# Kernel tuning notes

Hardware: AMD Instinct MI355X
Metric: run time of the kernel (lower is better)

## Reference

```python
import jax, jax.numpy as jnp
import numpy as np

N_NODES = 50000
N_EDGES = 1600000
N_DECODE = 500000
D = 128
EPS = 1e-6


def _sage_conv(x, src, dst, Wl, bl, Wr, n_nodes):
    # PyG SAGEConv (mean aggr): out = lin_l(mean_{j in N(i)} x_j) + lin_r(x_i)
    msg = x[src]                                            # [E, D] gather
    s = jax.ops.segment_sum(msg, dst, num_segments=n_nodes) # [N, D]
    cnt = jax.ops.segment_sum(jnp.ones((src.shape[0],), x.dtype), dst,
                              num_segments=n_nodes)         # [N]
    aggr = s / jnp.maximum(cnt, 1.0)[:, None]
    return aggr @ Wl + bl + x @ Wr


def setup_inputs() -> dict:
    key = jax.random.key(0)
    ks = jax.random.split(key, 9)
    scale = 1.0 / np.sqrt(D)
    x = jax.random.normal(ks[0], (N_NODES, D), dtype=jnp.float32)
    edge_index = jax.random.randint(ks[1], (2, N_EDGES), 0, N_NODES, dtype=jnp.int64)
    decode_index = jax.random.randint(ks[2], (2, N_DECODE), 0, N_NODES, dtype=jnp.int64)
    W1l = jax.random.normal(ks[3], (D, D), dtype=jnp.float32) * scale
    b1 = jnp.zeros((D,), dtype=jnp.float32)
    W1r = jax.random.normal(ks[4], (D, D), dtype=jnp.float32) * scale
    W2l = jax.random.normal(ks[5], (D, D), dtype=jnp.float32) * scale
    b2 = jnp.zeros((D,), dtype=jnp.float32)
    W2r = jax.random.normal(ks[6], (D, D), dtype=jnp.float32) * scale
    return {"x": x, "edge_index": edge_index, "decode_index": decode_index,
            "W1l": W1l, "b1": b1, "W1r": W1r, "W2l": W2l, "b2": b2, "W2r": W2r}


def reference(x, edge_index, decode_index, W1l, b1, W1r, W2l, b2, W2r):
    src, dst = edge_index[0], edge_index[1]
    h = _sage_conv(x, src, dst, W1l, b1, W1r, N_NODES)
    h = jax.nn.relu(h)
    # dropout is a no-op in eval mode (training=False)
    h = _sage_conv(h, src, dst, W2l, b2, W2r, N_NODES)
    a = h[decode_index[0]]                                  # [Dk, D]
    b = h[decode_index[1]]
    num = jnp.sum(a * b, axis=1)
    denom = jnp.maximum(jnp.linalg.norm(a, axis=1) * jnp.linalg.norm(b, axis=1), EPS)
    return jax.nn.sigmoid(num / denom)
```

## Files before the change

### kernel.cpp

```cpp
#include <hip/hip_runtime.h>
#include <cstddef>

#define D 128
#define NBITS 7
#define BCAP2 6144
#define CHUNK 4096
#define BSTRIDE8 36
#define DNPP 8

typedef float floatx4 __attribute__((ext_vector_type(4)));
typedef float floatx2 __attribute__((ext_vector_type(2)));

__device__ __forceinline__ int incl_scan64(int v) {
    const int lane = threadIdx.x & 63;
#pragma unroll
    for (int o = 1; o < 64; o <<= 1) {
        int u = __shfl_up(v, o);
        if (lane >= o) v += u;
    }
    return v;
}

__device__ __forceinline__ void accf8p(floatx2* a2, uint4 u) {
    unsigned w[4] = {u.x, u.y, u.z, u.w};
#pragma unroll
    for (int k = 0; k < 4; ++k) {
        a2[2 * k + 0] += __builtin_amdgcn_cvt_pk_f32_fp8((int)w[k], false);
        a2[2 * k + 1] += __builtin_amdgcn_cvt_pk_f32_fp8((int)w[k], true);
    }
}

__device__ __forceinline__ float dotf8(uint4 ua, uint4 ub) {
    unsigned wa[4] = {ua.x, ua.y, ua.z, ua.w};
    unsigned wb[4] = {ub.x, ub.y, ub.z, ub.w};
    float dot = 0.f;
#pragma unroll
    for (int k = 0; k < 4; ++k) {
        floatx2 alo = __builtin_amdgcn_cvt_pk_f32_fp8((int)wa[k], false);
        floatx2 ahi = __builtin_amdgcn_cvt_pk_f32_fp8((int)wa[k], true);
        floatx2 blo = __builtin_amdgcn_cvt_pk_f32_fp8((int)wb[k], false);
        floatx2 bhi = __builtin_amdgcn_cvt_pk_f32_fp8((int)wb[k], true);
        dot = fmaf(alo.x, blo.x, dot);
        dot = fmaf(alo.y, blo.y, dot);
        dot = fmaf(ahi.x, bhi.x, dot);
        dot = fmaf(ahi.y, bhi.y, dot);
    }
    return dot;
}

__global__ void __launch_bounds__(256) k1_prep_bucket(
        const float* __restrict__ x, unsigned* __restrict__ xf8,
        int nq, int nblk_a,
        const float* __restrict__ W1l, const float* __restrict__ W1r,
        const float* __restrict__ W2l, const float* __restrict__ W2r,
        unsigned* __restrict__ Wtf8,
        const int* __restrict__ src, const int* __restrict__ dst, int n_edges,
        unsigned* __restrict__ chunk_data, int* __restrict__ chunk_off,
        int nbuck) {
    int blk = (int)blockIdx.x;
    const int tid = threadIdx.x;
    if (blk < nblk_a) {
        int t = blk * 256 + tid;
        if (t < nq) {
            float4 v = ((const float4*)x)[t];
            int lo = __builtin_amdgcn_cvt_pk_fp8_f32(v.x, v.y, 0, false);
            xf8[t] = (unsigned)__builtin_amdgcn_cvt_pk_fp8_f32(v.z, v.w, lo, true);
        }
        return;
    }
    blk -= nblk_a;
    if (blk < 64) {
        int t2 = blk * 256 + tid;
        int widx = t2 >> 12;
        int within = t2 & 4095;
        int n = within >> 5;
        int g = within & 31;
        const float* W = (widx == 0) ? W1l : (widx == 1) ? W1r : (widx == 2) ? W2l : W2r;
        float w0 = W[(size_t)(4 * g + 0) * D + n];
        float w1 = W[(size_t)(4 * g + 1) * D + n];
        float w2 = W[(size_t)(4 * g + 2) * D + n];
        float w3 = W[(size_t)(4 * g + 3) * D + n];
        int lo = __builtin_amdgcn_cvt_pk_fp8_f32(w0, w1, 0, false);
        Wtf8[(size_t)widx * 4096 + (size_t)n * 32 + g] =
            (unsigned)__builtin_amdgcn_cvt_pk_fp8_f32(w2, w3, lo, true);
        return;
    }
    blk -= 64;
    __shared__ int cnt[512];
    __shared__ int cur[512];
    __shared__ int wsum[4];
    __shared__ unsigned ent[CHUNK];
    const int c = blk;
    const int e0 = c * CHUNK;
    const int n = min(CHUNK, n_edges - e0);
    cnt[tid] = 0;
    cnt[tid + 256] = 0;
    __syncthreads();
    for (int i = tid; i < n; i += 256)
        atomicAdd(&cnt[dst[e0 + i] >> NBITS], 1);
    __syncthreads();
    int c0 = cnt[2 * tid], c1 = cnt[2 * tid + 1];
    int v = c0 + c1;
    int s = incl_scan64(v);
    if ((tid & 63) == 63) wsum[tid >> 6] = s;
    __syncthreads();
    {
        int wv = tid >> 6;
        int add = (wv > 0 ? wsum[0] : 0) + (wv > 1 ? wsum[1] : 0) + (wv > 2 ? wsum[2] : 0);
        int excl = s + add - v;
        cur[2 * tid] = excl;
        cur[2 * tid + 1] = excl + c0;
        const size_t base = (size_t)c * (nbuck + 1);
        if (2 * tid <= nbuck) chunk_off[base + 2 * tid] = excl;
        if (2 * tid + 1 <= nbuck) chunk_off[base + 2 * tid + 1] = excl + c0;
    }
    __syncthreads();
    for (int i = tid; i < n; i += 256) {
        int d = dst[e0 + i];
        int sv = src[e0 + i];
        int b = d >> NBITS;
        int p = atomicAdd(&cur[b], 1);
        ent[p] = ((unsigned)(d & ((1 << NBITS) - 1)) << 16) | (unsigned)sv;
    }
    __syncthreads();
    for (int i = tid; i < n; i += 256) chunk_data[(size_t)e0 + i] = ent[i];
}

__global__ void __launch_bounds__(512) k2_csr(
        const unsigned* __restrict__ chunk_data, const int* __restrict__ chunk_off,
        int nchunk, int nbuck,
        unsigned* __restrict__ csr16g, int* __restrict__ offsG,
        int* __restrict__ degG) {
    __shared__ unsigned short lcsr[BCAP2];
    __shared__ int ndeg[128], ncur[128];
    __shared__ int s_w0, s_tot;
    const int tid = threadIdx.x;
    const int b = blockIdx.x;
    const int stride = nbuck + 1;

    if (tid < 128) ndeg[tid] = 0;
    __syncthreads();

    const int w = tid >> 1, half = tid & 1;
    for (int c = w; c < nchunk; c += 256) {
        int beg = chunk_off[(size_t)c * stride + b];
        int end = chunk_off[(size_t)c * stride + b + 1];
        const unsigned* cd = chunk_data + (size_t)c * CHUNK;
        for (int i = beg + half; i < end; i += 2)
            atomicAdd(&ndeg[cd[i] >> 16], 1);
    }
    __syncthreads();
    int v = 0, pd = 0, s = 0;
    if (tid < 128) {
        v = ndeg[tid];
        pd = (v + 7) & ~7;
        s = incl_scan64(pd);
        if (tid == 63) s_w0 = s;
    }
    __syncthreads();
    if (tid < 128) {
        if (tid >= 64) s += s_w0;
        int excl = min(s - pd, BCAP2);
        int de = v;
        if (excl + de > BCAP2) de = max(0, BCAP2 - excl);
        ncur[tid] = excl;
        offsG[(size_t)b * 128 + tid] = excl;
        degG[(size_t)b * 128 + tid] = de;
        if (tid == 127) s_tot = min(s, BCAP2);
    }
    __syncthreads();
    for (int c = w; c < nchunk; c += 256) {
        int beg = chunk_off[(size_t)c * stride + b];
        int end = chunk_off[(size_t)c * stride + b + 1];
        const unsigned* cd = chunk_data + (size_t)c * CHUNK;
        for (int i = beg + half; i < end; i += 2) {
            unsigned e = cd[i];
            int pos = atomicAdd(&ncur[e >> 16], 1);
            if (pos < BCAP2) lcsr[pos] = (unsigned short)(e & 0xffffu);
        }
    }
    __syncthreads();
    {
        int tot = s_tot;
        int words = (tot + 1) >> 1;
        const unsigned* l32 = (const unsigned*)lcsr;
        for (int i = tid; i < words; i += 512)
            csr16g[(size_t)b * (BCAP2 / 2) + i] = l32[i];
    }
}

__global__ void __launch_bounds__(256, 6) gather_hi(
        const unsigned* __restrict__ feat,
        const int* __restrict__ offsG, const int* __restrict__ degG,
        const unsigned* __restrict__ csr16g,
        unsigned* __restrict__ agg, int n_nodes) {
    const int wid = (blockIdx.x * blockDim.x + threadIdx.x) >> 6;
    const int lane = threadIdx.x & 63;
    const int q = lane >> 3;
    const int l8 = lane & 7;
    const int node = wid * 8 + q;
    const int nc = (node < n_nodes) ? node : (n_nodes - 1);
    const unsigned short* csr = (const unsigned short*)csr16g
                                + (size_t)(nc >> NBITS) * BCAP2;
    const int beg = offsG[nc];
    const int de  = degG[nc];
    const int end = beg + de;
    const unsigned* fb = feat + (size_t)l8 * 4;
    floatx2 a2[8];
#pragma unroll
    for (int i = 0; i < 8; ++i) a2[i] = (floatx2)(0.f);
    int e = beg;
    for (; e + 8 <= end; e += 8) {
        uint4 idv = *(const uint4*)(csr + e);
        unsigned id0 = idv.x & 0xffffu, id1 = idv.x >> 16;
        unsigned id2 = idv.y & 0xffffu, id3 = idv.y >> 16;
        unsigned id4 = idv.z & 0xffffu, id5 = idv.z >> 16;
        unsigned id6 = idv.w & 0xffffu, id7 = idv.w >> 16;
        uint4 u0 = *(const uint4*)(fb + (size_t)id0 * 32);
        uint4 u1 = *(const uint4*)(fb + (size_t)id1 * 32);
        uint4 u2 = *(const uint4*)(fb + (size_t)id2 * 32);
        uint4 u3 = *(const uint4*)(fb + (size_t)id3 * 32);
        uint4 u4 = *(const uint4*)(fb + (size_t)id4 * 32);
        uint4 u5 = *(const uint4*)(fb + (size_t)id5 * 32);
        uint4 u6 = *(const uint4*)(fb + (size_t)id6 * 32);
        uint4 u7 = *(const uint4*)(fb + (size_t)id7 * 32);
        accf8p(a2, u0); accf8p(a2, u1); accf8p(a2, u2); accf8p(a2, u3);
        accf8p(a2, u4); accf8p(a2, u5); accf8p(a2, u6); accf8p(a2, u7);
    }
    for (; e < end; ++e) {
        uint4 u0 = *(const uint4*)(fb + (size_t)csr[e] * 32);
        accf8p(a2, u0);
    }
    float r = 1.0f / fmaxf((float)de, 1.0f);
    unsigned o[4];
#pragma unroll
    for (int j = 0; j < 4; ++j) {
        int lo = __builtin_amdgcn_cvt_pk_fp8_f32(a2[2 * j].x * r, a2[2 * j].y * r, 0, false);
        o[j] = (unsigned)__builtin_amdgcn_cvt_pk_fp8_f32(a2[2 * j + 1].x * r,
                                                         a2[2 * j + 1].y * r, lo, true);
    }
    if (node < n_nodes)
        *(uint4*)(agg + (size_t)node * 32 + l8 * 4) = make_uint4(o[0], o[1], o[2], o[3]);
}

__global__ void __launch_bounds__(256, 4) gemm128(
        const unsigned* __restrict__ aggf8, const unsigned* __restrict__ xin8,
        const unsigned* __restrict__ Wt, const float* __restrict__ bias,
        unsigned char* __restrict__ outf8, float* __restrict__ nrm2,
        int n_nodes, int relu) {
    __shared__ unsigned sB[2][128 * BSTRIDE8];
    const int tid = threadIdx.x;
    for (int i = tid; i < 2048; i += 256) {
        int m = i >> 10;
        int col = (i >> 3) & 127;
        int c4 = (i & 7) * 4;
        *(uint4*)&sB[m][col * BSTRIDE8 + c4] =
            *(const uint4*)(Wt + (size_t)m * 4096 + (size_t)col * 32 + c4);
    }
    __syncthreads();

    const int lane = tid & 63;
    const int wv = tid >> 6;
    const int li = lane & 15;
    const int quad = lane >> 4;
    const int node0 = blockIdx.x * 64 + wv * 16;
    if (node0 >= n_nodes) return;

    floatx4 acc[8];
#pragma unroll
    for (int t = 0; t < 8; ++t) acc[t] = (floatx4)(0.f);

    int arow = node0 + li;
    if (arow >= n_nodes) arow = n_nodes - 1;
    const unsigned* ap = aggf8 + (size_t)arow * 32 + quad * 2;
    const unsigned* xp = xin8 + (size_t)arow * 32 + quad * 2;
    const unsigned* sb0 = &sB[0][li * BSTRIDE8 + quad * 2];
    const unsigned* sb1 = &sB[1][li * BSTRIDE8 + quad * 2];

#pragma unroll
    for (int ks = 0; ks < 4; ++ks) {
        long af = *(const long*)(ap + ks * 8);
#pragma unroll
        for (int ct = 0; ct < 8; ++ct) {
            long bf = *(const long*)(sb0 + ct * 16 * BSTRIDE8 + ks * 8);
            acc[ct] = __builtin_amdgcn_mfma_f32_16x16x32_fp8_fp8(af, bf, acc[ct], 0, 0, 0);
        }
    }
#pragma unroll
    for (int ks = 0; ks < 4; ++ks) {
        long af = *(const long*)(xp + ks * 8);
#pragma unroll
        for (int ct = 0; ct < 8; ++ct) {
            long bf = *(const long*)(sb1 + ct * 16 * BSTRIDE8 + ks * 8);
            acc[ct] = __builtin_amdgcn_mfma_f32_16x16x32_fp8_fp8(af, bf, acc[ct], 0, 0, 0);
        }
    }
    float sq[4] = {0.f, 0.f, 0.f, 0.f};
#pragma unroll
    for (int ct = 0; ct < 8; ++ct) {
        int col = ct * 16 + li;
        float bv = bias[col];
#pragma unroll
        for (int r2 = 0; r2 < 4; ++r2) {
            int node2 = node0 + quad * 4 + r2;
            float o = acc[ct][r2] + bv;
            if (relu) o = fmaxf(o, 0.f);
            int pk = __builtin_amdgcn_cvt_pk_fp8_f32(o, o, 0, false);
            if (nrm2) {
                floatx2 dq = __builtin_amdgcn_cvt_pk_f32_fp8(pk, false);
                sq[r2] += dq.x * dq.x;
            }
            if (node2 < n_nodes)
                outf8[(size_t)node2 * D + col] = (unsigned char)(pk & 0xff);
        }
    }
    if (nrm2) {
#pragma unroll
        for (int r2 = 0; r2 < 4; ++r2) {
            float sv = sq[r2];
            sv += __shfl_xor(sv, 1);
            sv += __shfl_xor(sv, 2);
            sv += __shfl_xor(sv, 4);
            sv += __shfl_xor(sv, 8);
            int node2 = node0 + quad * 4 + r2;
            if (li == 0 && node2 < n_nodes) nrm2[node2] = sv;
        }
    }
}

__global__ void __launch_bounds__(256, 4) k5_decode(
        const unsigned* __restrict__ h2, const float* __restrict__ nrm2,
        const int* __restrict__ ia, const int* __restrict__ ib,
        float* __restrict__ out, int n_pairs) {
    const int tid = threadIdx.x;
    const int l8 = tid & 7;
    const int g = blockIdx.x * 32 + (tid >> 3);
    const int strideP = gridDim.x * 32;
    int pa[DNPP], pb[DNPP];
#pragma unroll
    for (int i = 0; i < DNPP; ++i) {
        int p = g + i * strideP;
        int pc = (p < n_pairs) ? p : 0;
        pa[i] = ia[pc];
        pb[i] = ib[pc];
    }
    uint4 ua[DNPP], ub[DNPP];
#pragma unroll
    for (int i = 0; i < DNPP; ++i) {
        ua[i] = *(const uint4*)(h2 + (size_t)pa[i] * 32 + l8 * 4);
        ub[i] = *(const uint4*)(h2 + (size_t)pb[i] * 32 + l8 * 4);
    }
#pragma unroll
    for (int i = 0; i < DNPP; ++i) {
        float dot = dotf8(ua[i], ub[i]);
        dot += __shfl_xor(dot, 1);
        dot += __shfl_xor(dot, 2);
        dot += __shfl_xor(dot, 4);
        int p = g + i * strideP;
        if (l8 == 0 && p < n_pairs) {
            float denom = fmaxf(sqrtf(nrm2[pa[i]] * nrm2[pb[i]]), 1e-6f);
            float s = dot / denom;
            out[p] = 1.0f / (1.0f + expf(-s));
        }
    }
}


extern "C" void kernel_launch(void* const* d_in, const int* in_sizes, int n_in,
                              void* d_out, int out_size, void* d_ws, size_t ws_size,
                              hipStream_t stream) {
    const float* x   = (const float*)d_in[0];
    const int*   ei  = (const int*)d_in[1];
    const int*   di  = (const int*)d_in[2];
    const float* W1l = (const float*)d_in[3];
    const float* b1  = (const float*)d_in[4];
    const float* W1r = (const float*)d_in[5];
    const float* W2l = (const float*)d_in[6];
    const float* b2  = (const float*)d_in[7];
    const float* W2r = (const float*)d_in[8];

    const int N = in_sizes[0] / D;
    const int E = in_sizes[1] / 2;
    const int K = in_sizes[2] / 2;
    const size_t NQ = (size_t)N * 32;
    const int NBUCK = (N + (1 << NBITS) - 1) >> NBITS;
    const int NCHUNK = (E + CHUNK - 1) / CHUNK;

    const int* src  = ei;
    const int* dstp = ei + E;
    const int* dia  = di;
    const int* dib  = di + K;

    unsigned* ws         = (unsigned*)d_ws;
    unsigned* chunk_data = ws;
    int*      chunk_off  = (int*)(chunk_data + E);
    unsigned* csr16g     = (unsigned*)(chunk_off + (size_t)NCHUNK * (NBUCK + 1));
    int*      offsG      = (int*)(csr16g + (size_t)NBUCK * (BCAP2 / 2));
    int*      degG       = offsG + (size_t)NBUCK * 128;
    float*    nrm2       = (float*)(degG + (size_t)NBUCK * 128);
    unsigned* Wtf8       = (unsigned*)(nrm2 + N);
    unsigned* xf8        = Wtf8 + 16384;
    unsigned* h1f8       = xf8 + NQ;
    unsigned* h2f8       = h1f8 + NQ;
    unsigned* aggf8      = h2f8 + NQ;

    float* out = (float*)d_out;

    const int nq = (int)NQ;
    const int nblk_a = (nq + 255) / 256;

    k1_prep_bucket<<<nblk_a + 64 + NCHUNK, 256, 0, stream>>>(
        x, xf8, nq, nblk_a, W1l, W1r, W2l, W2r, Wtf8,
        src, dstp, E, chunk_data, chunk_off, NBUCK);

    k2_csr<<<NBUCK, 512, 0, stream>>>(
        chunk_data, chunk_off, NCHUNK, NBUCK, csr16g, offsG, degG);

    const int gather_blocks = ((N + 7) / 8 + 3) / 4;
    const int gemm_blocks = (N + 63) / 64;

    gather_hi<<<gather_blocks, 256, 0, stream>>>(xf8, offsG, degG, csr16g, aggf8, N);
    gemm128<<<gemm_blocks, 256, 0, stream>>>(aggf8, xf8, Wtf8, b1,
                                             (unsigned char*)h1f8, nullptr, N, 1);

    gather_hi<<<gather_blocks, 256, 0, stream>>>(h1f8, offsG, degG, csr16g, aggf8, N);
    gemm128<<<gemm_blocks, 256, 0, stream>>>(aggf8, h1f8, Wtf8 + 8192, b2,
                                             (unsigned char*)h2f8, nrm2, N, 0);

    {
        int G = (K + 32 * DNPP - 1) / (32 * DNPP);
        k5_decode<<<G, 256, 0, stream>>>(h2f8, nrm2, dia, dib, out, K);
    }
}
```

Measured before the change: 239.9 us.

## Split fp8 feature matrices into two 64-column planes for cache-resident gathers

Stores the fp8 node features (x, h1, h2, agg) as two column planes of 64 bytes per node instead of 128-byte rows. The gather and decode kernels now run once per plane, so each pass touches a 3.2 MB working set that fits better in cache during random neighbor access. The GEMM reads and writes the planar layout, and decode accumulates a partial dot product across two launches. The cost is extra kernel launches, re-reading the CSR indices and decode indices twice, and a byte-strided output store in the GEMM.

```diff
diff --git a/kernel.cpp b/kernel.cpp
--- a/kernel.cpp
+++ b/kernel.cpp
@@ -50,7 +50,7 @@
 
 __global__ void __launch_bounds__(256) k1_prep_bucket(
         const float* __restrict__ x, unsigned* __restrict__ xf8,
-        int nq, int nblk_a,
+        int nq, int nblk_a, int N16,
         const float* __restrict__ W1l, const float* __restrict__ W1r,
         const float* __restrict__ W2l, const float* __restrict__ W2r,
         unsigned* __restrict__ Wtf8,
@@ -64,7 +64,9 @@
         if (t < nq) {
             float4 v = ((const float4*)x)[t];
             int lo = __builtin_amdgcn_cvt_pk_fp8_f32(v.x, v.y, 0, false);
-            xf8[t] = (unsigned)__builtin_amdgcn_cvt_pk_fp8_f32(v.z, v.w, lo, true);
+            unsigned w = (unsigned)__builtin_amdgcn_cvt_pk_fp8_f32(v.z, v.w, lo, true);
+            int n = t >> 5, j = t & 31;
+            xf8[(size_t)(j >> 4) * N16 + (size_t)n * 16 + (j & 15)] = w;
         }
         return;
     }
@@ -189,23 +191,23 @@
     }
 }
 
-__global__ void __launch_bounds__(256, 6) gather_hi(
-        const unsigned* __restrict__ feat,
+__global__ void __launch_bounds__(256, 4) gather_plane(
+        const unsigned* __restrict__ featp,
         const int* __restrict__ offsG, const int* __restrict__ degG,
         const unsigned* __restrict__ csr16g,
-        unsigned* __restrict__ agg, int n_nodes) {
+        unsigned* __restrict__ aggp, int n_nodes) {
     const int wid = (blockIdx.x * blockDim.x + threadIdx.x) >> 6;
     const int lane = threadIdx.x & 63;
-    const int q = lane >> 3;
-    const int l8 = lane & 7;
-    const int node = wid * 8 + q;
+    const int q = lane >> 2;
+    const int l4 = lane & 3;
+    const int node = wid * 16 + q;
     const int nc = (node < n_nodes) ? node : (n_nodes - 1);
     const unsigned short* csr = (const unsigned short*)csr16g
                                 + (size_t)(nc >> NBITS) * BCAP2;
     const int beg = offsG[nc];
     const int de  = degG[nc];
     const int end = beg + de;
-    const unsigned* fb = feat + (size_t)l8 * 4;
+    const unsigned* fb = featp + (size_t)l4 * 4;
     floatx2 a2[8];
 #pragma unroll
     for (int i = 0; i < 8; ++i) a2[i] = (floatx2)(0.f);
@@ -216,19 +218,19 @@
         unsigned id2 = idv.y & 0xffffu, id3 = idv.y >> 16;
         unsigned id4 = idv.z & 0xffffu, id5 = idv.z >> 16;
         unsigned id6 = idv.w & 0xffffu, id7 = idv.w >> 16;
-        uint4 u0 = *(const uint4*)(fb + (size_t)id0 * 32);
-        uint4 u1 = *(const uint4*)(fb + (size_t)id1 * 32);
-        uint4 u2 = *(const uint4*)(fb + (size_t)id2 * 32);
-        uint4 u3 = *(const uint4*)(fb + (size_t)id3 * 32);
-        uint4 u4 = *(const uint4*)(fb + (size_t)id4 * 32);
-        uint4 u5 = *(const uint4*)(fb + (size_t)id5 * 32);
-        uint4 u6 = *(const uint4*)(fb + (size_t)id6 * 32);
-        uint4 u7 = *(const uint4*)(fb + (size_t)id7 * 32);
+        uint4 u0 = *(const uint4*)(fb + (size_t)id0 * 16);
+        uint4 u1 = *(const uint4*)(fb + (size_t)id1 * 16);
+        uint4 u2 = *(const uint4*)(fb + (size_t)id2 * 16);
+        uint4 u3 = *(const uint4*)(fb + (size_t)id3 * 16);
+        uint4 u4 = *(const uint4*)(fb + (size_t)id4 * 16);
+        uint4 u5 = *(const uint4*)(fb + (size_t)id5 * 16);
+        uint4 u6 = *(const uint4*)(fb + (size_t)id6 * 16);
+        uint4 u7 = *(const uint4*)(fb + (size_t)id7 * 16);
         accf8p(a2, u0); accf8p(a2, u1); accf8p(a2, u2); accf8p(a2, u3);
         accf8p(a2, u4); accf8p(a2, u5); accf8p(a2, u6); accf8p(a2, u7);
     }
     for (; e < end; ++e) {
-        uint4 u0 = *(const uint4*)(fb + (size_t)csr[e] * 32);
+        uint4 u0 = *(const uint4*)(fb + (size_t)csr[e] * 16);
         accf8p(a2, u0);
     }
     float r = 1.0f / fmaxf((float)de, 1.0f);
@@ -240,14 +242,14 @@
                                                          a2[2 * j + 1].y * r, lo, true);
     }
     if (node < n_nodes)
-        *(uint4*)(agg + (size_t)node * 32 + l8 * 4) = make_uint4(o[0], o[1], o[2], o[3]);
+        *(uint4*)(aggp + (size_t)node * 16 + l4 * 4) = make_uint4(o[0], o[1], o[2], o[3]);
 }
 
 __global__ void __launch_bounds__(256, 4) gemm128(
         const unsigned* __restrict__ aggf8, const unsigned* __restrict__ xin8,
         const unsigned* __restrict__ Wt, const float* __restrict__ bias,
         unsigned char* __restrict__ outf8, float* __restrict__ nrm2,
-        int n_nodes, int relu) {
+        int n_nodes, int N16, int relu) {
     __shared__ unsigned sB[2][128 * BSTRIDE8];
     const int tid = threadIdx.x;
     for (int i = tid; i < 2048; i += 256) {
@@ -272,14 +274,14 @@
 
     int arow = node0 + li;
     if (arow >= n_nodes) arow = n_nodes - 1;
-    const unsigned* ap = aggf8 + (size_t)arow * 32 + quad * 2;
-    const unsigned* xp = xin8 + (size_t)arow * 32 + quad * 2;
+    const unsigned* ap = aggf8 + (size_t)arow * 16 + quad * 2;
+    const unsigned* xp = xin8 + (size_t)arow * 16 + quad * 2;
     const unsigned* sb0 = &sB[0][li * BSTRIDE8 + quad * 2];
     const unsigned* sb1 = &sB[1][li * BSTRIDE8 + quad * 2];
 
 #pragma unroll
     for (int ks = 0; ks < 4; ++ks) {
-        long af = *(const long*)(ap + ks * 8);
+        long af = *(const long*)(ap + (size_t)(ks >> 1) * N16 + (ks & 1) * 8);
 #pragma unroll
         for (int ct = 0; ct < 8; ++ct) {
             long bf = *(const long*)(sb0 + ct * 16 * BSTRIDE8 + ks * 8);
@@ -288,7 +290,7 @@
     }
 #pragma unroll
     for (int ks = 0; ks < 4; ++ks) {
-        long af = *(const long*)(xp + ks * 8);
+        long af = *(const long*)(xp + (size_t)(ks >> 1) * N16 + (ks & 1) * 8);
 #pragma unroll
         for (int ct = 0; ct < 8; ++ct) {
             long bf = *(const long*)(sb1 + ct * 16 * BSTRIDE8 + ks * 8);
@@ -300,6 +302,7 @@
     for (int ct = 0; ct < 8; ++ct) {
         int col = ct * 16 + li;
         float bv = bias[col];
+        unsigned char* hp = outf8 + (size_t)(col >> 6) * ((size_t)N16 * 4) + (col & 63);
 #pragma unroll
         for (int r2 = 0; r2 < 4; ++r2) {
             int node2 = node0 + quad * 4 + r2;
@@ -311,7 +314,7 @@
                 sq[r2] += dq.x * dq.x;
             }
             if (node2 < n_nodes)
-                outf8[(size_t)node2 * D + col] = (unsigned char)(pk & 0xff);
+                hp[(size_t)node2 * 64] = (unsigned char)(pk & 0xff);
         }
     }
     if (nrm2) {
@@ -328,14 +331,16 @@
     }
 }
 
-__global__ void __launch_bounds__(256, 4) k5_decode(
-        const unsigned* __restrict__ h2, const float* __restrict__ nrm2,
+__global__ void __launch_bounds__(256, 4) decode_plane(
+        const unsigned* __restrict__ h2p,
+        const float* __restrict__ nrm2,
         const int* __restrict__ ia, const int* __restrict__ ib,
-        float* __restrict__ out, int n_pairs) {
+        float* __restrict__ partial, float* __restrict__ out,
+        int n_pairs, int finalp) {
     const int tid = threadIdx.x;
-    const int l8 = tid & 7;
-    const int g = blockIdx.x * 32 + (tid >> 3);
-    const int strideP = gridDim.x * 32;
+    const int l4 = tid & 3;
+    const int g = blockIdx.x * 64 + (tid >> 2);
+    const int strideP = gridDim.x * 64;
     int pa[DNPP], pb[DNPP];
 #pragma unroll
     for (int i = 0; i < DNPP; ++i) {
@@ -344,23 +349,28 @@
         pa[i] = ia[pc];
         pb[i] = ib[pc];
     }
+    const unsigned* hb = h2p + (size_t)l4 * 4;
     uint4 ua[DNPP], ub[DNPP];
 #pragma unroll
     for (int i = 0; i < DNPP; ++i) {
-        ua[i] = *(const uint4*)(h2 + (size_t)pa[i] * 32 + l8 * 4);
-        ub[i] = *(const uint4*)(h2 + (size_t)pb[i] * 32 + l8 * 4);
+        ua[i] = *(const uint4*)(hb + (size_t)pa[i] * 16);
+        ub[i] = *(const uint4*)(hb + (size_t)pb[i] * 16);
     }
 #pragma unroll
     for (int i = 0; i < DNPP; ++i) {
         float dot = dotf8(ua[i], ub[i]);
         dot += __shfl_xor(dot, 1);
         dot += __shfl_xor(dot, 2);
-        dot += __shfl_xor(dot, 4);
         int p = g + i * strideP;
-        if (l8 == 0 && p < n_pairs) {
-            float denom = fmaxf(sqrtf(nrm2[pa[i]] * nrm2[pb[i]]), 1e-6f);
-            float s = dot / denom;
-            out[p] = 1.0f / (1.0f + expf(-s));
+        if (l4 == 0 && p < n_pairs) {
+            if (!finalp) {
+                partial[p] = dot;
+            } else {
+                dot += partial[p];
+                float denom = fmaxf(sqrtf(nrm2[pa[i]] * nrm2[pb[i]]), 1e-6f);
+                float s = dot / denom;
+                out[p] = 1.0f / (1.0f + expf(-s));
+            }
         }
     }
 }
@@ -382,6 +392,7 @@
     const int N = in_sizes[0] / D;
     const int E = in_sizes[1] / 2;
     const int K = in_sizes[2] / 2;
+    const int N16 = N * 16;
     const size_t NQ = (size_t)N * 32;
     const int NBUCK = (N + (1 << NBITS) - 1) >> NBITS;
     const int NCHUNK = (E + CHUNK - 1) / CHUNK;
@@ -403,6 +414,7 @@
     unsigned* h1f8       = xf8 + NQ;
     unsigned* h2f8       = h1f8 + NQ;
     unsigned* aggf8      = h2f8 + NQ;
+    float*    partial    = (float*)chunk_data;
 
     float* out = (float*)d_out;
 
@@ -410,25 +422,34 @@
     const int nblk_a = (nq + 255) / 256;
 
     k1_prep_bucket<<<nblk_a + 64 + NCHUNK, 256, 0, stream>>>(
-        x, xf8, nq, nblk_a, W1l, W1r, W2l, W2r, Wtf8,
+        x, xf8, nq, nblk_a, N16, W1l, W1r, W2l, W2r, Wtf8,
         src, dstp, E, chunk_data, chunk_off, NBUCK);
 
     k2_csr<<<NBUCK, 512, 0, stream>>>(
         chunk_data, chunk_off, NCHUNK, NBUCK, csr16g, offsG, degG);
 
-    const int gather_blocks = ((N + 7) / 8 + 3) / 4;
+    const int gather_blocks = (((N + 15) / 16) + 3) / 4;
     const int gemm_blocks = (N + 63) / 64;
 
-    gather_hi<<<gather_blocks, 256, 0, stream>>>(xf8, offsG, degG, csr16g, aggf8, N);
+    gather_plane<<<gather_blocks, 256, 0, stream>>>(
+        xf8, offsG, degG, csr16g, aggf8, N);
+    gather_plane<<<gather_blocks, 256, 0, stream>>>(
+        xf8 + (size_t)N16, offsG, degG, csr16g, aggf8 + (size_t)N16, N);
     gemm128<<<gemm_blocks, 256, 0, stream>>>(aggf8, xf8, Wtf8, b1,
-                                             (unsigned char*)h1f8, nullptr, N, 1);
-
-    gather_hi<<<gather_blocks, 256, 0, stream>>>(h1f8, offsG, degG, csr16g, aggf8, N);
+                                             (unsigned char*)h1f8, nullptr, N, N16, 1);
+
+    gather_plane<<<gather_blocks, 256, 0, stream>>>(
+        h1f8, offsG, degG, csr16g, aggf8, N);
+    gather_plane<<<gather_blocks, 256, 0, stream>>>(
+        h1f8 + (size_t)N16, offsG, degG, csr16g, aggf8 + (size_t)N16, N);
     gemm128<<<gemm_blocks, 256, 0, stream>>>(aggf8, h1f8, Wtf8 + 8192, b2,
-                                             (unsigned char*)h2f8, nrm2, N, 0);
+                                             (unsigned char*)h2f8, nrm2, N, N16, 0);
 
     {
-        int G = (K + 32 * DNPP - 1) / (32 * DNPP);
-        k5_decode<<<G, 256, 0, stream>>>(h2f8, nrm2, dia, dib, out, K);
-    }
-}
+        int G = (K + 64 * DNPP - 1) / (64 * DNPP);
+        decode_plane<<<G, 256, 0, stream>>>(h2f8, nrm2, dia, dib,
+                                            partial, out, K, 0);
+        decode_plane<<<G, 256, 0, stream>>>(h2f8 + (size_t)N16, nrm2, dia, dib,
+                                            partial, out, K, 1);
+    }
+}
```

Measured after the change: 253.1 us. +5.5%, slower.
